# Optimization experiments

Hardware: AMD Instinct MI355X
Metric: run time of the kernel (lower is better)

Reference implementation:

```python
import jax, jax.numpy as jnp
import numpy as np

B, S, D = 2, 2048, 1024
E, K, F = 64, 6, 1408
DFF = 4096
N = B * S
CAP = 768
Z_LOSS_W = 1e-6
MOE_SCALE = 0.5  # 1/(1 + (num_shared_experts > 0))


def setup_inputs() -> dict:
    key = jax.random.key(0)
    ks = jax.random.split(key, 7)
    x = jax.random.normal(ks[0], (B, S, D), jnp.float32)
    router_w = jax.random.normal(ks[1], (E, D), jnp.float32) * 0.01
    experts_w12 = jax.random.normal(ks[2], (E, D, 2 * F), jnp.float32) * 0.011
    experts_w3 = jax.random.normal(ks[3], (E, F, D), jnp.float32) * 0.011
    gate_w = jax.random.normal(ks[4], (DFF, D), jnp.float32) * 0.011
    up_w = jax.random.normal(ks[5], (DFF, D), jnp.float32) * 0.011
    down_w = jax.random.normal(ks[6], (D, DFF), jnp.float32) * 0.011
    return {"x": x, "router_w": router_w, "experts_w12": experts_w12,
            "experts_w3": experts_w3, "gate_w": gate_w, "up_w": up_w,
            "down_w": down_w}


def reference(x, router_w, experts_w12, experts_w3, gate_w, up_w, down_w):
    b, s, d = x.shape
    h = x.reshape(-1, d)                    # [N, D]
    n = h.shape[0]

    # ---- router (fp32) ----
    logits = h @ router_w.T                 # [N, E]
    scores = jax.nn.sigmoid(logits)
    z_loss = jnp.mean(logits ** 2) * Z_LOSS_W
    # expert_bias defaults to zeros -> selection on scores directly
    _, topk_idx = jax.lax.top_k(scores, K)  # [N, K]
    topk_idx = jnp.clip(topk_idx, 0, E - 1)
    topk_logits = jnp.take_along_axis(logits, topk_idx, axis=1)
    gating = jax.nn.softmax(topk_logits, axis=-1).astype(jnp.bfloat16)  # [N, K]

    # ---- shared expert (dense SwiGLU) ----
    shared = (jax.nn.silu(h @ gate_w.T) * (h @ up_w.T)) @ down_w.T  # [N, D]

    # ---- dispatch: sort token-expert pairs by expert, scatter into padded buffer ----
    flat_idx = topk_idx.reshape(-1)                     # [N*K]
    order = jnp.argsort(flat_idx)
    expert_sorted = flat_idx[order]                     # [N*K]
    token_ids = jnp.repeat(jnp.arange(n), K)[order]     # source token per pair
    counts = jnp.bincount(flat_idx, length=E)
    starts = jnp.concatenate([jnp.zeros((1,), counts.dtype), jnp.cumsum(counts)[:-1]])
    intra = jnp.arange(n * K) - starts[expert_sorted]   # slot within expert
    valid = intra < CAP
    dest = jnp.where(valid, expert_sorted * CAP + intra, E * CAP)  # overflow -> trash row

    grouped = h[token_ids]                              # [N*K, D]
    padded = jnp.zeros((E * CAP + 1, d), h.dtype).at[dest].set(grouped)
    padded = padded[:-1].reshape(E, CAP, d)             # [E, CAP, D]

    # ---- per-expert grouped GEMM (SwiGLU) ----
    h12 = jnp.einsum('ecd,edf->ecf', padded, experts_w12)   # [E, CAP, 2F]
    h1, h2 = jnp.split(h12, 2, axis=-1)
    act = jax.nn.silu(h1) * h2
    eout = jnp.einsum('ecf,efd->ecd', act, experts_w3)      # [E, CAP, D]

    # ---- combine: gather back and scatter-add into token order ----
    eout_flat = jnp.concatenate([eout.reshape(-1, d), jnp.zeros((1, d), eout.dtype)])
    full = eout_flat[dest]                              # [N*K, D]
    g_sorted = gating.reshape(-1)[order].astype(h.dtype)
    weighted = full * g_sorted[:, None]
    routed = jnp.zeros((n, d), h.dtype).at[token_ids].add(weighted)

    # eval mode: aux_loss = 0, route_scale = 1.0
    out = (shared + routed) * MOE_SCALE
    return out.reshape(b, s, d), z_loss
```

## Files before the change

kernel.cpp:

```cpp
#include <hip/hip_runtime.h>
#include <stdint.h>
#include <math.h>

#define NTOK 4096
#define DIM  1024
#define NEXP 64
#define KSEL 6
#define FF   1408
#define FF2  2816
#define DFFC 4096
#define CAPE 768

typedef __bf16 bf16x8 __attribute__((ext_vector_type(8)));
typedef float  f32x4  __attribute__((ext_vector_type(4)));

__device__ __forceinline__ float bf2f(uint32_t h) {
  union { uint32_t u; float f; } v; v.u = h << 16; return v.f;
}
__device__ __forceinline__ uint16_t f2bf(float f) {
  union { float f; uint32_t u; } v; v.f = f;
  return (uint16_t)((v.u + 0x7fffu + ((v.u >> 16) & 1u)) >> 16);
}
__device__ __forceinline__ uint32_t pk_bf16(float a, float b) {
  uint32_t r;
  asm("v_cvt_pk_bf16_f32 %0, %1, %2" : "=v"(r) : "v"(a), "v"(b));
  return r;
}
__device__ __forceinline__ int swzh(int r) { return ((r ^ (r >> 2)) & 7) << 3; }

__device__ __forceinline__ void load_lds16(const void* g, void* l) {
  __builtin_amdgcn_global_load_lds((const __attribute__((address_space(1))) void*)g,
                                   (__attribute__((address_space(3))) void*)l, 16, 0, 0);
}

__global__ __launch_bounds__(256) void router_kernel(const float* __restrict__ x,
                                                     const float* __restrict__ rw,
                                                     int* __restrict__ topk,
                                                     uint16_t* __restrict__ gating,
                                                     float* __restrict__ tokz,
                                                     uint16_t* __restrict__ hb) {
  __shared__ float hs[16 * DIM];
  __shared__ float lg[16][NEXP];
  const int tid = threadIdx.x;
  const int t0 = blockIdx.x * 16;
  const float4* xin = (const float4*)(x + (size_t)t0 * DIM);
  float4* hs4 = (float4*)hs;
  for (int i = tid; i < 16 * DIM / 4; i += 256) hs4[i] = xin[i];
  __syncthreads();
  {
    ushort4* hbo = (ushort4*)(hb + (size_t)t0 * DIM);
    for (int i = tid; i < 16 * DIM / 4; i += 256) {
      float4 v = hs4[i];
      ushort4 o;
      o.x = f2bf(v.x); o.y = f2bf(v.y); o.z = f2bf(v.z); o.w = f2bf(v.w);
      hbo[i] = o;
    }
  }
  const int e = tid >> 2, q = tid & 3;
  float part[16];
#pragma unroll
  for (int tt = 0; tt < 16; tt++) part[tt] = 0.f;
  const float4* rw4 = (const float4*)(rw + (size_t)e * DIM + q * 256);
  for (int i = 0; i < 64; i++) {
    float4 w = rw4[i];
#pragma unroll
    for (int tt = 0; tt < 16; tt++) {
      float4 h = *(const float4*)(hs + tt * DIM + q * 256 + i * 4);
      part[tt] += h.x * w.x + h.y * w.y + h.z * w.z + h.w * w.w;
    }
  }
#pragma unroll
  for (int tt = 0; tt < 16; tt++) {
    float v = part[tt];
    v += __shfl_xor(v, 1);
    v += __shfl_xor(v, 2);
    if (q == 0) lg[tt][e] = v;
  }
  __syncthreads();
  const int wid = tid >> 6, lane = tid & 63;
  for (int ti = 0; ti < 4; ti++) {
    int tt = wid * 4 + ti;
    float v = lg[tt][lane];
    float z = v * v;
#pragma unroll
    for (int off = 32; off; off >>= 1) z += __shfl_xor(z, off);
    float bv[KSEL]; int bi[KSEL];
#pragma unroll
    for (int s = 0; s < KSEL; s++) {
      float m = v; int mi = lane;
#pragma unroll
      for (int off = 32; off; off >>= 1) {
        float om = __shfl_xor(m, off); int oi = __shfl_xor(mi, off);
        if (om > m || (om == m && oi < mi)) { m = om; mi = oi; }
      }
      bv[s] = m; bi[s] = mi;
      if (lane == mi) v = -3.0e38f;
    }
    if (lane == 0) {
      int t = t0 + tt;
      tokz[t] = z;
      float mx = bv[0];
      float ex[KSEL], sum = 0.f;
#pragma unroll
      for (int s = 0; s < KSEL; s++) { ex[s] = expf(bv[s] - mx); sum += ex[s]; }
      float inv = 1.f / sum;
#pragma unroll
      for (int s = 0; s < KSEL; s++) {
        topk[t * KSEL + s] = bi[s];
        gating[t * KSEL + s] = f2bf(ex[s] * inv);
      }
    }
  }
}

__global__ __launch_bounds__(256) void zred_kernel(const float* __restrict__ tz,
                                                   float* __restrict__ out) {
  __shared__ float s[256];
  float a = 0.f;
  for (int i = threadIdx.x; i < NTOK; i += 256) a += tz[i];
  s[threadIdx.x] = a; __syncthreads();
  for (int st = 128; st; st >>= 1) {
    if (threadIdx.x < (unsigned)st) s[threadIdx.x] += s[threadIdx.x + st];
    __syncthreads();
  }
  if (threadIdx.x == 0) out[0] = s[0] * (1e-6f / ((float)NTOK * (float)NEXP));
}

__global__ __launch_bounds__(64) void dispatch_kernel(const int* __restrict__ topk,
                                                      int* __restrict__ dest,
                                                      int* __restrict__ invmap,
                                                      int* __restrict__ counts) {
  const int e = blockIdx.x;
  const int lane = threadIdx.x;
  int base = 0;
  for (int it = 0; it < (NTOK * KSEL) / 64; it++) {
    int p = it * 64 + lane;
    int ex = topk[p];
    bool m = (ex == e);
    unsigned long long mask = __ballot(m);
    if (m) {
      int intra = base + __popcll(mask & ((1ull << lane) - 1ull));
      if (intra < CAPE) {
        dest[p] = e * CAPE + intra;
        invmap[e * CAPE + intra] = p / KSEL;
      } else {
        dest[p] = -1;
      }
    }
    base += __popcll(mask);
  }
  if (lane == 0) counts[e] = base < CAPE ? base : CAPE;
}

#define BM 128
#define BN 128
#define BKK 64

template<int EPI, int BSRC, bool IND, bool REMAP>
__global__ __launch_bounds__(256, 2) void gemm_f(const uint16_t* __restrict__ A,
                                                 const float* __restrict__ B,
                                                 const float* __restrict__ B2,
                                                 void* __restrict__ C,
                                                 const int* __restrict__ invmap,
                                                 const int* __restrict__ counts,
                                                 int K, int lda, int ldb, int ldc,
                                                 long long strideA, long long strideB,
                                                 long long strideC, int grouped,
                                                 int nM, int nN) {
  const int per = gridDim.x >> 3;
  const int w = ((int)blockIdx.x & 7) * per + ((int)blockIdx.x >> 3);
  const int mi = w % nM;
  const int q1 = w / nM;
  const int ni = q1 % nN;
  const int e  = q1 / nN;
  int cnt = 1 << 30;
  if (grouped) {
    cnt = counts[e];
    if (mi * BM >= cnt) return;
  }
  const int bm0 = mi * BM, bn0 = ni * BN;
  const uint16_t* Ab = A + (size_t)e * strideA;
  const float* Bb = B + (size_t)e * strideB;
  __shared__ alignas(16) uint16_t sA[BM * BKK];
  __shared__ alignas(16) uint16_t sB[BN * BKK];
  const int tid = threadIdx.x, wid = tid >> 6, lane = tid & 63;

  const int sa = tid >> 3;
  const int colk = (((tid & 7) ^ ((sa ^ (sa >> 2)) & 7)) * 8);
  const uint16_t* ap[4];
#pragma unroll
  for (int i = 0; i < 4; i++) {
    int row = i * 32 + sa;
    int ar = bm0 + row;
    if constexpr (IND) {
      int cr = ar < cnt ? ar : (cnt - 1);
      ar = invmap[e * CAPE + cr];
    }
    ap[i] = Ab + (size_t)ar * lda + colk;
  }

  const float* bpa = nullptr;
  const float* bpb = nullptr;
  if constexpr (BSRC == 1) {
    const int kc = (tid & 15) * 4;
    bpa = Bb + (size_t)(bn0 + (tid >> 4)) * ldb + kc;
  } else if constexpr (BSRC == 3) {
    const int kc = (tid & 15) * 4;
    const int gcol = (bn0 >> 1) + (tid >> 4);
    bpa = B  + (size_t)gcol * ldb + kc;
    bpb = B2 + (size_t)gcol * ldb + kc;
  } else {
    const int n0 = 4 * (tid & 31);
    int vn0 = bn0 + n0;
    int ng0;
    if constexpr (REMAP) {
      int blk = vn0 >> 5, lo = vn0 & 31;
      ng0 = blk * 16 + (lo & 15) + (lo < 16 ? 0 : FF);
    } else {
      ng0 = vn0;
    }
    bpa = Bb + (size_t)(4 * (tid >> 5)) * ldb + ng0;
  }

  f32x4 zero = {0.f, 0.f, 0.f, 0.f};
  f32x4 acc[4][4];
#pragma unroll
  for (int i = 0; i < 4; i++)
#pragma unroll
    for (int j = 0; j < 4; j++) acc[i][j] = zero;
  const int wm = wid >> 1, wn = wid & 1;

  for (int k0 = 0; k0 < K; k0 += BKK) {
#pragma unroll
    for (int i = 0; i < 4; i++) {
      load_lds16(ap[i], sA + i * 2048 + wid * 512);
      ap[i] += BKK;
    }
    f32x4 v[8];
    if constexpr (BSRC == 1) {
#pragma unroll
      for (int it = 0; it < 8; it++)
        v[it] = *(const f32x4*)(bpa + (size_t)(it * 16) * ldb);
      bpa += BKK;
    } else if constexpr (BSRC == 3) {
#pragma unroll
      for (int it = 0; it < 8; it++) {
        const float* s = (it & 1) ? bpb : bpa;
        v[it] = *(const f32x4*)(s + (size_t)((it >> 1) * 16) * ldb);
      }
      bpa += BKK; bpb += BKK;
    } else {
#pragma unroll
      for (int i2 = 0; i2 < 2; i2++)
#pragma unroll
        for (int j = 0; j < 4; j++)
          v[i2 * 4 + j] = *(const f32x4*)(bpa + (size_t)(32 * i2 + j) * ldb);
      bpa += (size_t)BKK * ldb;
    }
    if constexpr (BSRC == 1 || BSRC == 3) {
      const int kc = (tid & 15) * 4;
#pragma unroll
      for (int it = 0; it < 8; it++) {
        int nr = (tid >> 4) + it * 16;
        uint2 p;
        p.x = pk_bf16(v[it][0], v[it][1]);
        p.y = pk_bf16(v[it][2], v[it][3]);
        *(uint2*)(sB + nr * BKK + (kc ^ swzh(nr))) = p;
      }
    } else {
      const int n0 = 4 * (tid & 31);
#pragma unroll
      for (int i2 = 0; i2 < 2; i2++) {
        int kk0 = 4 * (tid >> 5) + 32 * i2;
#pragma unroll
        for (int c = 0; c < 4; c++) {
          int nr = n0 + c;
          uint2 p;
          p.x = pk_bf16(v[i2 * 4 + 0][c], v[i2 * 4 + 1][c]);
          p.y = pk_bf16(v[i2 * 4 + 2][c], v[i2 * 4 + 3][c]);
          *(uint2*)(sB + nr * BKK + (kk0 ^ swzh(nr))) = p;
        }
      }
    }
    __syncthreads();
#pragma unroll
    for (int ks = 0; ks < 2; ks++) {
      const int kb = ks * 32 + (lane >> 4) * 8;
      bf16x8 af[4], bfr[4];
#pragma unroll
      for (int f = 0; f < 4; f++) {
        int rowA = wm * 64 + f * 16 + (lane & 15);
        af[f] = *(const bf16x8*)(sA + rowA * BKK + (kb ^ swzh(rowA)));
      }
#pragma unroll
      for (int f = 0; f < 4; f++) {
        int rowB = wn * 64 + f * 16 + (lane & 15);
        bfr[f] = *(const bf16x8*)(sB + rowB * BKK + (kb ^ swzh(rowB)));
      }
#pragma unroll
      for (int fm = 0; fm < 4; fm++)
#pragma unroll
        for (int fn = 0; fn < 4; fn++)
          acc[fm][fn] = __builtin_amdgcn_mfma_f32_16x16x32_bf16(af[fm], bfr[fn],
                                                                acc[fm][fn], 0, 0, 0);
    }
    __syncthreads();
  }

  const int lr = (lane >> 4) * 4, lc = lane & 15;
  if constexpr (EPI == 2) {
    uint16_t* outp = (uint16_t*)C + (size_t)e * strideC;
#pragma unroll
    for (int fm = 0; fm < 4; fm++) {
#pragma unroll
      for (int fp = 0; fp < 2; fp++) {
        f32x4 g = acc[fm][2 * fp], u = acc[fm][2 * fp + 1];
        int fcol = (bn0 >> 1) + wn * 32 + fp * 16 + lc;
#pragma unroll
        for (int j = 0; j < 4; j++) {
          int r = bm0 + wm * 64 + fm * 16 + lr + j;
          float gv = g[j];
          float sv = (gv / (1.f + expf(-gv))) * u[j];
          outp[(size_t)r * ldc + fcol] = f2bf(sv);
        }
      }
    }
  } else if constexpr (EPI == 1) {
    float* outp = (float*)C + (size_t)e * strideC;
#pragma unroll
    for (int fm = 0; fm < 4; fm++)
#pragma unroll
      for (int fn = 0; fn < 4; fn++) {
        int col = bn0 + wn * 64 + fn * 16 + lc;
#pragma unroll
        for (int j = 0; j < 4; j++) {
          int r = bm0 + wm * 64 + fm * 16 + lr + j;
          outp[(size_t)r * ldc + col] = acc[fm][fn][j];
        }
      }
  } else {
    uint16_t* outp = (uint16_t*)C + (size_t)e * strideC;
#pragma unroll
    for (int fm = 0; fm < 4; fm++)
#pragma unroll
      for (int fn = 0; fn < 4; fn++) {
        int col = bn0 + wn * 64 + fn * 16 + lc;
#pragma unroll
        for (int j = 0; j < 4; j++) {
          int r = bm0 + wm * 64 + fm * 16 + lr + j;
          outp[(size_t)r * ldc + col] = f2bf(acc[fm][fn][j]);
        }
      }
  }
}

__global__ __launch_bounds__(256) void combine_kernel(const float* __restrict__ shout,
                                                      const uint16_t* __restrict__ eout,
                                                      const int* __restrict__ dest,
                                                      const uint16_t* __restrict__ gating,
                                                      float* __restrict__ out) {
  const int t = blockIdx.x;
  const int d0 = threadIdx.x * 4;
  float4 sh = *(const float4*)(shout + (size_t)t * DIM + d0);
  float rx = 0.f, ry = 0.f, rz = 0.f, rw = 0.f;
#pragma unroll
  for (int k = 0; k < KSEL; k++) {
    int dp = dest[t * KSEL + k];
    if (dp >= 0) {
      float gw = bf2f(gating[t * KSEL + k]);
      ushort4 ev = *(const ushort4*)(eout + (size_t)dp * DIM + d0);
      rx += gw * bf2f(ev.x);
      ry += gw * bf2f(ev.y);
      rz += gw * bf2f(ev.z);
      rw += gw * bf2f(ev.w);
    }
  }
  float4 o;
  o.x = (sh.x + rx) * 0.5f;
  o.y = (sh.y + ry) * 0.5f;
  o.z = (sh.z + rz) * 0.5f;
  o.w = (sh.w + rw) * 0.5f;
  *(float4*)(out + (size_t)t * DIM + d0) = o;
}

extern "C" void kernel_launch(void* const* d_in, const int* in_sizes, int n_in,
                              void* d_out, int out_size, void* d_ws, size_t ws_size,
                              hipStream_t stream) {
  (void)in_sizes; (void)n_in; (void)out_size; (void)ws_size;
  const float* x   = (const float*)d_in[0];
  const float* rw  = (const float*)d_in[1];
  const float* w12 = (const float*)d_in[2];
  const float* w3  = (const float*)d_in[3];
  const float* gw  = (const float*)d_in[4];
  const float* uw  = (const float*)d_in[5];
  const float* dw  = (const float*)d_in[6];
  float* out = (float*)d_out;

  char* ws = (char*)d_ws;
  size_t off = 0;
  auto alloc = [&](size_t sz) -> void* {
    void* p = ws + off;
    off += (sz + 255) & ~(size_t)255;
    return p;
  };
  uint16_t* HB    = (uint16_t*)alloc((size_t)NTOK * DIM * 2);
  uint16_t* S1    = (uint16_t*)alloc((size_t)NTOK * DFFC * 2);
  uint16_t* ACT   = (uint16_t*)alloc((size_t)NEXP * CAPE * FF * 2);
  uint16_t* EOUT  = (uint16_t*)alloc((size_t)NEXP * CAPE * DIM * 2);
  float* SHOUT    = (float*)alloc((size_t)NTOK * DIM * 4);
  int* TOPKB      = (int*)alloc((size_t)NTOK * KSEL * 4);
  uint16_t* GATING= (uint16_t*)alloc((size_t)NTOK * KSEL * 2);
  int* DEST       = (int*)alloc((size_t)NTOK * KSEL * 4);
  int* INVMAP     = (int*)alloc((size_t)NEXP * CAPE * 4);
  int* COUNTS     = (int*)alloc((size_t)NEXP * 4);
  float* TOKZ     = (float*)alloc((size_t)NTOK * 4);

  router_kernel<<<NTOK / 16, 256, 0, stream>>>(x, rw, TOPKB, GATING, TOKZ, HB);
  dispatch_kernel<<<NEXP, 64, 0, stream>>>(TOPKB, DEST, INVMAP, COUNTS);
  zred_kernel<<<1, 256, 0, stream>>>(TOKZ, out + (size_t)NTOK * DIM);

  gemm_f<2, 3, false, false><<<(NTOK / BM) * (2 * DFFC / BN), 256, 0, stream>>>(
      HB, gw, uw, S1, nullptr, nullptr, DIM, DIM, DIM, DFFC, 0, 0, 0, 0,
      NTOK / BM, 2 * DFFC / BN);
  gemm_f<1, 1, false, false><<<(NTOK / BM) * (DIM / BN), 256, 0, stream>>>(
      S1, dw, nullptr, SHOUT, nullptr, nullptr, DFFC, DFFC, DFFC, DIM, 0, 0, 0, 0,
      NTOK / BM, DIM / BN);

  gemm_f<2, 2, true, true><<<(CAPE / BM) * (FF2 / BN) * NEXP, 256, 0, stream>>>(
      HB, w12, nullptr, ACT, INVMAP, COUNTS, DIM, DIM, FF2, FF,
      0, (long long)DIM * FF2, (long long)CAPE * FF, 1, CAPE / BM, FF2 / BN);
  gemm_f<0, 2, false, false><<<(CAPE / BM) * (DIM / BN) * NEXP, 256, 0, stream>>>(
      ACT, w3, nullptr, EOUT, nullptr, COUNTS, FF, FF, DIM, DIM,
      (long long)CAPE * FF, (long long)FF * DIM, (long long)CAPE * DIM, 1,
      CAPE / BM, DIM / BN);

  combine_kernel<<<NTOK, 256, 0, stream>>>(SHOUT, EOUT, DEST, GATING, out);
}
```

Before: 854.0 us.

## Double-buffer LDS tiles in GEMM kernel to overlap loads with MFMA

Splits the shared-memory A and B tiles into two buffers. The next K-slice's global loads (fp32 B into registers, async A into LDS) are issued before the MFMA work on the current buffer, and B is converted and written into the other buffer afterwards. This drops one of the two barriers per iteration and hides global memory latency behind compute. The cost is twice the LDS use and more live registers, which may lower occupancy.

```diff
diff --git a/kernel.cpp b/kernel.cpp
--- a/kernel.cpp
+++ b/kernel.cpp
@@ -181,8 +181,8 @@
   const int bm0 = mi * BM, bn0 = ni * BN;
   const uint16_t* Ab = A + (size_t)e * strideA;
   const float* Bb = B + (size_t)e * strideB;
-  __shared__ alignas(16) uint16_t sA[BM * BKK];
-  __shared__ alignas(16) uint16_t sB[BN * BKK];
+  __shared__ alignas(16) uint16_t sA[2][BM * BKK];
+  __shared__ alignas(16) uint16_t sB[2][BN * BKK];
   const int tid = threadIdx.x, wid = tid >> 6, lane = tid & 63;
 
   const int sa = tid >> 3;
@@ -222,21 +222,7 @@
     bpa = Bb + (size_t)(4 * (tid >> 5)) * ldb + ng0;
   }
 
-  f32x4 zero = {0.f, 0.f, 0.f, 0.f};
-  f32x4 acc[4][4];
-#pragma unroll
-  for (int i = 0; i < 4; i++)
-#pragma unroll
-    for (int j = 0; j < 4; j++) acc[i][j] = zero;
-  const int wm = wid >> 1, wn = wid & 1;
-
-  for (int k0 = 0; k0 < K; k0 += BKK) {
-#pragma unroll
-    for (int i = 0; i < 4; i++) {
-      load_lds16(ap[i], sA + i * 2048 + wid * 512);
-      ap[i] += BKK;
-    }
-    f32x4 v[8];
+  auto loadB = [&](f32x4 (&v)[8]) {
     if constexpr (BSRC == 1) {
 #pragma unroll
       for (int it = 0; it < 8; it++)
@@ -257,6 +243,15 @@
           v[i2 * 4 + j] = *(const f32x4*)(bpa + (size_t)(32 * i2 + j) * ldb);
       bpa += (size_t)BKK * ldb;
     }
+  };
+  auto issueA = [&](int buf) {
+#pragma unroll
+    for (int i = 0; i < 4; i++) {
+      load_lds16(ap[i], sA[buf] + i * 2048 + wid * 512);
+      ap[i] += BKK;
+    }
+  };
+  auto writeB = [&](int buf, f32x4 (&v)[8]) {
     if constexpr (BSRC == 1 || BSRC == 3) {
       const int kc = (tid & 15) * 4;
 #pragma unroll
@@ -265,7 +260,7 @@
         uint2 p;
         p.x = pk_bf16(v[it][0], v[it][1]);
         p.y = pk_bf16(v[it][2], v[it][3]);
-        *(uint2*)(sB + nr * BKK + (kc ^ swzh(nr))) = p;
+        *(uint2*)(sB[buf] + nr * BKK + (kc ^ swzh(nr))) = p;
       }
     } else {
       const int n0 = 4 * (tid & 31);
@@ -278,11 +273,37 @@
           uint2 p;
           p.x = pk_bf16(v[i2 * 4 + 0][c], v[i2 * 4 + 1][c]);
           p.y = pk_bf16(v[i2 * 4 + 2][c], v[i2 * 4 + 3][c]);
-          *(uint2*)(sB + nr * BKK + (kk0 ^ swzh(nr))) = p;
+          *(uint2*)(sB[buf] + nr * BKK + (kk0 ^ swzh(nr))) = p;
         }
       }
     }
-    __syncthreads();
+  };
+
+  f32x4 zero = {0.f, 0.f, 0.f, 0.f};
+  f32x4 acc[4][4];
+#pragma unroll
+  for (int i = 0; i < 4; i++)
+#pragma unroll
+    for (int j = 0; j < 4; j++) acc[i][j] = zero;
+  const int wm = wid >> 1, wn = wid & 1;
+
+  {
+    f32x4 v[8];
+    loadB(v);
+    issueA(0);
+    writeB(0, v);
+  }
+  __syncthreads();
+
+  const int T = K / BKK;
+  for (int t = 0; t < T; t++) {
+    const int cur = t & 1;
+    const bool more = (t + 1 < T);
+    f32x4 v[8];
+    if (more) {
+      loadB(v);
+      issueA(cur ^ 1);
+    }
 #pragma unroll
     for (int ks = 0; ks < 2; ks++) {
       const int kb = ks * 32 + (lane >> 4) * 8;
@@ -290,12 +311,12 @@
 #pragma unroll
       for (int f = 0; f < 4; f++) {
         int rowA = wm * 64 + f * 16 + (lane & 15);
-        af[f] = *(const bf16x8*)(sA + rowA * BKK + (kb ^ swzh(rowA)));
+        af[f] = *(const bf16x8*)(sA[cur] + rowA * BKK + (kb ^ swzh(rowA)));
       }
 #pragma unroll
       for (int f = 0; f < 4; f++) {
         int rowB = wn * 64 + f * 16 + (lane & 15);
-        bfr[f] = *(const bf16x8*)(sB + rowB * BKK + (kb ^ swzh(rowB)));
+        bfr[f] = *(const bf16x8*)(sB[cur] + rowB * BKK + (kb ^ swzh(rowB)));
       }
 #pragma unroll
       for (int fm = 0; fm < 4; fm++)
@@ -304,6 +325,7 @@
           acc[fm][fn] = __builtin_amdgcn_mfma_f32_16x16x32_bf16(af[fm], bfr[fn],
                                                                 acc[fm][fn], 0, 0, 0);
     }
+    if (more) writeB(cur ^ 1, v);
     __syncthreads();
   }
 
```

After: 866.3 us. Within noise of the previous version (+1.4%).

## Replace GEMM with 256x256 eight-wave double-buffered phased pipeline kernel

Applied to the files above, without the earlier changes.

Replaces the 128x128, 4-wave single-buffered GEMM with a 256x256-tile, 512-thread kernel that double-buffers LDS for A and B. The K loop is split into four phases that interleave the next stage's global loads, LDS writes and async A copies with MFMA work, using barriers, waitcnt and s_setprio. The goal is more operand reuse per tile and hiding memory latency behind MFMA. In exchange, the larger LDS footprint and register use lower occupancy, and the grouped expert GEMMs waste more work on partially filled 256-row tiles.

```diff
diff --git a/kernel.cpp b/kernel.cpp
--- a/kernel.cpp
+++ b/kernel.cpp
@@ -152,21 +152,19 @@
   if (lane == 0) counts[e] = base < CAPE ? base : CAPE;
 }
 
-#define BM 128
-#define BN 128
 #define BKK 64
 
 template<int EPI, int BSRC, bool IND, bool REMAP>
-__global__ __launch_bounds__(256, 2) void gemm_f(const uint16_t* __restrict__ A,
-                                                 const float* __restrict__ B,
-                                                 const float* __restrict__ B2,
-                                                 void* __restrict__ C,
-                                                 const int* __restrict__ invmap,
-                                                 const int* __restrict__ counts,
-                                                 int K, int lda, int ldb, int ldc,
-                                                 long long strideA, long long strideB,
-                                                 long long strideC, int grouped,
-                                                 int nM, int nN) {
+__global__ __launch_bounds__(512, 2) void gemm8(const uint16_t* __restrict__ A,
+                                                const float* __restrict__ B,
+                                                const float* __restrict__ B2,
+                                                void* __restrict__ C,
+                                                const int* __restrict__ invmap,
+                                                const int* __restrict__ counts,
+                                                int K, int lda, int ldb, int ldc,
+                                                long long strideA, long long strideB,
+                                                long long strideC, int grouped,
+                                                int nM, int nN) {
   const int per = gridDim.x >> 3;
   const int w = ((int)blockIdx.x & 7) * per + ((int)blockIdx.x >> 3);
   const int mi = w % nM;
@@ -176,149 +174,212 @@
   int cnt = 1 << 30;
   if (grouped) {
     cnt = counts[e];
-    if (mi * BM >= cnt) return;
-  }
-  const int bm0 = mi * BM, bn0 = ni * BN;
+    if (mi * 256 >= cnt) return;
+  }
+  const int bm0 = mi * 256, bn0 = ni * 256;
   const uint16_t* Ab = A + (size_t)e * strideA;
   const float* Bb = B + (size_t)e * strideB;
-  __shared__ alignas(16) uint16_t sA[BM * BKK];
-  __shared__ alignas(16) uint16_t sB[BN * BKK];
+  __shared__ alignas(16) uint16_t sA[2][256 * 64];
+  __shared__ alignas(16) uint16_t sB[2][256 * 64];
   const int tid = threadIdx.x, wid = tid >> 6, lane = tid & 63;
-
-  const int sa = tid >> 3;
-  const int colk = (((tid & 7) ^ ((sa ^ (sa >> 2)) & 7)) * 8);
-  const uint16_t* ap[4];
-#pragma unroll
-  for (int i = 0; i < 4; i++) {
-    int row = i * 32 + sa;
-    int ar = bm0 + row;
-    if constexpr (IND) {
-      int cr = ar < cnt ? ar : (cnt - 1);
-      ar = invmap[e * CAPE + cr];
-    }
-    ap[i] = Ab + (size_t)ar * lda + colk;
-  }
-
-  const float* bpa = nullptr;
-  const float* bpb = nullptr;
+  const int wm = wid >> 2, wn = wid & 3;
+  const int l15 = lane & 15, q8 = (lane >> 4) * 8;
+
+  const uint16_t* apg[4];
+#pragma unroll
+  for (int h = 0; h < 2; h++)
+#pragma unroll
+    for (int i = 0; i < 2; i++) {
+      int R = h * 128 + i * 64 + (tid >> 3);
+      int ar = bm0 + R;
+      if constexpr (IND) {
+        int cr = ar < cnt ? ar : cnt - 1;
+        ar = invmap[e * CAPE + cr];
+      }
+      apg[h * 2 + i] = Ab + (size_t)ar * lda + (((tid & 7) ^ ((R ^ (R >> 2)) & 7)) * 8);
+    }
+
+  const float* bp[2];
+  long long bstep;
   if constexpr (BSRC == 1) {
-    const int kc = (tid & 15) * 4;
-    bpa = Bb + (size_t)(bn0 + (tid >> 4)) * ldb + kc;
+#pragma unroll
+    for (int h = 0; h < 2; h++) {
+      int n = bn0 + h * 128 + (tid >> 2);
+      bp[h] = Bb + (size_t)n * ldb + (tid & 3) * 16;
+    }
+    bstep = BKK;
   } else if constexpr (BSRC == 3) {
-    const int kc = (tid & 15) * 4;
-    const int gcol = (bn0 >> 1) + (tid >> 4);
-    bpa = B  + (size_t)gcol * ldb + kc;
-    bpb = B2 + (size_t)gcol * ldb + kc;
+#pragma unroll
+    for (int h = 0; h < 2; h++) {
+      int vn = bn0 + h * 128 + (tid >> 2);
+      const float* s0 = ((vn & 31) < 16) ? B : B2;
+      int pn = (vn >> 5) * 16 + (vn & 15);
+      bp[h] = s0 + (size_t)pn * ldb + (tid & 3) * 16;
+    }
+    bstep = BKK;
   } else {
-    const int n0 = 4 * (tid & 31);
-    int vn0 = bn0 + n0;
-    int ng0;
-    if constexpr (REMAP) {
-      int blk = vn0 >> 5, lo = vn0 & 31;
-      ng0 = blk * 16 + (lo & 15) + (lo < 16 ? 0 : FF);
+#pragma unroll
+    for (int h = 0; h < 2; h++) {
+      int vn0 = bn0 + h * 128 + (tid & 31) * 4;
+      int ng0;
+      if constexpr (REMAP) {
+        int blk = vn0 >> 5, lo = vn0 & 31;
+        ng0 = blk * 16 + (lo & 15) + (lo < 16 ? 0 : FF);
+      } else {
+        ng0 = vn0;
+      }
+      bp[h] = Bb + (size_t)((tid >> 5) * 4) * ldb + ng0;
+    }
+    bstep = (long long)BKK * ldb;
+  }
+
+  auto stageLoad = [&](int h, f32x4 (&bv)[4]) {
+    if constexpr (BSRC == 2) {
+#pragma unroll
+      for (int j = 0; j < 4; j++) bv[j] = *(const f32x4*)(bp[h] + (size_t)j * ldb);
     } else {
-      ng0 = vn0;
-    }
-    bpa = Bb + (size_t)(4 * (tid >> 5)) * ldb + ng0;
-  }
-
-  f32x4 zero = {0.f, 0.f, 0.f, 0.f};
-  f32x4 acc[4][4];
-#pragma unroll
-  for (int i = 0; i < 4; i++)
-#pragma unroll
-    for (int j = 0; j < 4; j++) acc[i][j] = zero;
-  const int wm = wid >> 1, wn = wid & 1;
-
-  for (int k0 = 0; k0 < K; k0 += BKK) {
-#pragma unroll
-    for (int i = 0; i < 4; i++) {
-      load_lds16(ap[i], sA + i * 2048 + wid * 512);
-      ap[i] += BKK;
-    }
-    f32x4 v[8];
-    if constexpr (BSRC == 1) {
-#pragma unroll
-      for (int it = 0; it < 8; it++)
-        v[it] = *(const f32x4*)(bpa + (size_t)(it * 16) * ldb);
-      bpa += BKK;
-    } else if constexpr (BSRC == 3) {
-#pragma unroll
-      for (int it = 0; it < 8; it++) {
-        const float* s = (it & 1) ? bpb : bpa;
-        v[it] = *(const f32x4*)(s + (size_t)((it >> 1) * 16) * ldb);
-      }
-      bpa += BKK; bpb += BKK;
+#pragma unroll
+      for (int j = 0; j < 4; j++) bv[j] = *(const f32x4*)(bp[h] + 4 * j);
+    }
+    bp[h] += bstep;
+  };
+  auto stageWrite = [&](int nb, int h, f32x4 (&bv)[4]) {
+    if constexpr (BSRC == 2) {
+#pragma unroll
+      for (int c = 0; c < 4; c++) {
+        int R = h * 128 + (tid & 31) * 4 + c;
+        uint2 p;
+        p.x = pk_bf16(bv[0][c], bv[1][c]);
+        p.y = pk_bf16(bv[2][c], bv[3][c]);
+        *(uint2*)(&sB[nb][R * 64 + (((tid >> 5) * 4) ^ swzh(R))]) = p;
+      }
     } else {
-#pragma unroll
-      for (int i2 = 0; i2 < 2; i2++)
-#pragma unroll
-        for (int j = 0; j < 4; j++)
-          v[i2 * 4 + j] = *(const f32x4*)(bpa + (size_t)(32 * i2 + j) * ldb);
-      bpa += (size_t)BKK * ldb;
-    }
-    if constexpr (BSRC == 1 || BSRC == 3) {
-      const int kc = (tid & 15) * 4;
-#pragma unroll
-      for (int it = 0; it < 8; it++) {
-        int nr = (tid >> 4) + it * 16;
-        uint2 p;
-        p.x = pk_bf16(v[it][0], v[it][1]);
-        p.y = pk_bf16(v[it][2], v[it][3]);
-        *(uint2*)(sB + nr * BKK + (kc ^ swzh(nr))) = p;
-      }
-    } else {
-      const int n0 = 4 * (tid & 31);
-#pragma unroll
-      for (int i2 = 0; i2 < 2; i2++) {
-        int kk0 = 4 * (tid >> 5) + 32 * i2;
-#pragma unroll
-        for (int c = 0; c < 4; c++) {
-          int nr = n0 + c;
-          uint2 p;
-          p.x = pk_bf16(v[i2 * 4 + 0][c], v[i2 * 4 + 1][c]);
-          p.y = pk_bf16(v[i2 * 4 + 2][c], v[i2 * 4 + 3][c]);
-          *(uint2*)(sB + nr * BKK + (kk0 ^ swzh(nr))) = p;
-        }
-      }
-    }
-    __syncthreads();
-#pragma unroll
-    for (int ks = 0; ks < 2; ks++) {
-      const int kb = ks * 32 + (lane >> 4) * 8;
-      bf16x8 af[4], bfr[4];
-#pragma unroll
-      for (int f = 0; f < 4; f++) {
-        int rowA = wm * 64 + f * 16 + (lane & 15);
-        af[f] = *(const bf16x8*)(sA + rowA * BKK + (kb ^ swzh(rowA)));
-      }
-#pragma unroll
-      for (int f = 0; f < 4; f++) {
-        int rowB = wn * 64 + f * 16 + (lane & 15);
-        bfr[f] = *(const bf16x8*)(sB + rowB * BKK + (kb ^ swzh(rowB)));
-      }
-#pragma unroll
-      for (int fm = 0; fm < 4; fm++)
-#pragma unroll
-        for (int fn = 0; fn < 4; fn++)
-          acc[fm][fn] = __builtin_amdgcn_mfma_f32_16x16x32_bf16(af[fm], bfr[fn],
-                                                                acc[fm][fn], 0, 0, 0);
-    }
-    __syncthreads();
+      int R = h * 128 + (tid >> 2);
+      int s = swzh(R);
+      uint4 u;
+      u.x = pk_bf16(bv[0][0], bv[0][1]); u.y = pk_bf16(bv[0][2], bv[0][3]);
+      u.z = pk_bf16(bv[1][0], bv[1][1]); u.w = pk_bf16(bv[1][2], bv[1][3]);
+      *(uint4*)(&sB[nb][R * 64 + ((((tid & 3) * 16) + 0) ^ s)]) = u;
+      u.x = pk_bf16(bv[2][0], bv[2][1]); u.y = pk_bf16(bv[2][2], bv[2][3]);
+      u.z = pk_bf16(bv[3][0], bv[3][1]); u.w = pk_bf16(bv[3][2], bv[3][3]);
+      *(uint4*)(&sB[nb][R * 64 + ((((tid & 3) * 16) + 8) ^ s)]) = u;
+    }
+  };
+  auto stageA = [&](int nb, int h) {
+#pragma unroll
+    for (int i = 0; i < 2; i++) {
+      load_lds16(apg[h * 2 + i], &sA[nb][h * 8192 + i * 4096 + tid * 8]);
+      apg[h * 2 + i] += BKK;
+    }
+  };
+
+  f32x4 acc[8][4];
+#pragma unroll
+  for (int i = 0; i < 8; i++)
+#pragma unroll
+    for (int j = 0; j < 4; j++) acc[i][j] = (f32x4){0.f, 0.f, 0.f, 0.f};
+
+  auto readA = [&](int buf, int mh, int ks, bf16x8 (&af)[4]) {
+#pragma unroll
+    for (int f = 0; f < 4; f++) {
+      int R = wm * 128 + (mh * 4 + f) * 16 + l15;
+      af[f] = *(const bf16x8*)(&sA[buf][R * 64 + ((ks * 32 + q8) ^ swzh(R))]);
+    }
+  };
+  auto readB = [&](int buf, int ks, bf16x8 (&bq)[4]) {
+#pragma unroll
+    for (int f = 0; f < 4; f++) {
+      int R = wn * 64 + f * 16 + l15;
+      bq[f] = *(const bf16x8*)(&sB[buf][R * 64 + ((ks * 32 + q8) ^ swzh(R))]);
+    }
+  };
+
+#define MFMAQ(mh, af, bq)                                                      \
+  _Pragma("unroll") for (int f = 0; f < 4; f++)                                \
+  _Pragma("unroll") for (int n = 0; n < 4; n++)                                \
+    acc[(mh) * 4 + f][n] = __builtin_amdgcn_mfma_f32_16x16x32_bf16(            \
+        af[f], bq[n], acc[(mh) * 4 + f][n], 0, 0, 0);
+
+#define PH_GATE()                                                              \
+  __builtin_amdgcn_s_barrier();                                                \
+  asm volatile("s_waitcnt lgkmcnt(0)" ::: "memory");                           \
+  __builtin_amdgcn_sched_barrier(0);                                           \
+  __builtin_amdgcn_s_setprio(1);
+
+#define PH_END()                                                               \
+  __builtin_amdgcn_s_setprio(0);                                               \
+  __builtin_amdgcn_s_barrier();
+
+  {
+    f32x4 bv0[4], bv1[4];
+    stageLoad(0, bv0);
+    stageLoad(1, bv1);
+    stageA(0, 0);
+    stageA(0, 1);
+    stageWrite(0, 0, bv0);
+    stageWrite(0, 1, bv1);
+  }
+  asm volatile("s_waitcnt vmcnt(0) lgkmcnt(0)" ::: "memory");
+  __builtin_amdgcn_sched_barrier(0);
+  __builtin_amdgcn_s_barrier();
+
+  const int T = K / BKK;
+  for (int t = 0; t < T; t++) {
+    const int cur = t & 1, nb = cur ^ 1;
+    const bool more = (t + 1 < T);
+    bf16x8 bq[4];
+    f32x4 bv0[4], bv1[4];
+    {
+      bf16x8 af[4];
+      readA(cur, 0, 0, af);
+      readB(cur, 0, bq);
+      if (more) stageLoad(0, bv0);
+      PH_GATE();
+      MFMAQ(0, af, bq);
+      PH_END();
+    }
+    {
+      bf16x8 af[4];
+      readA(cur, 1, 0, af);
+      if (more) { stageLoad(1, bv1); stageA(nb, 0); }
+      PH_GATE();
+      MFMAQ(1, af, bq);
+      PH_END();
+    }
+    {
+      bf16x8 af[4];
+      readA(cur, 0, 1, af);
+      readB(cur, 1, bq);
+      if (more) { stageWrite(nb, 0, bv0); stageA(nb, 1); }
+      PH_GATE();
+      MFMAQ(0, af, bq);
+      PH_END();
+    }
+    {
+      bf16x8 af[4];
+      readA(cur, 1, 1, af);
+      if (more) stageWrite(nb, 1, bv1);
+      PH_GATE();
+      MFMAQ(1, af, bq);
+      __builtin_amdgcn_s_setprio(0);
+      asm volatile("s_waitcnt vmcnt(0)" ::: "memory");
+      __builtin_amdgcn_sched_barrier(0);
+      __builtin_amdgcn_s_barrier();
+    }
   }
 
   const int lr = (lane >> 4) * 4, lc = lane & 15;
   if constexpr (EPI == 2) {
     uint16_t* outp = (uint16_t*)C + (size_t)e * strideC;
 #pragma unroll
-    for (int fm = 0; fm < 4; fm++) {
+    for (int mf = 0; mf < 8; mf++) {
 #pragma unroll
       for (int fp = 0; fp < 2; fp++) {
-        f32x4 g = acc[fm][2 * fp], u = acc[fm][2 * fp + 1];
+        f32x4 g = acc[mf][2 * fp], u = acc[mf][2 * fp + 1];
         int fcol = (bn0 >> 1) + wn * 32 + fp * 16 + lc;
 #pragma unroll
         for (int j = 0; j < 4; j++) {
-          int r = bm0 + wm * 64 + fm * 16 + lr + j;
+          int r = bm0 + wm * 128 + mf * 16 + lr + j;
           float gv = g[j];
           float sv = (gv / (1.f + expf(-gv))) * u[j];
           outp[(size_t)r * ldc + fcol] = f2bf(sv);
@@ -328,30 +389,33 @@
   } else if constexpr (EPI == 1) {
     float* outp = (float*)C + (size_t)e * strideC;
 #pragma unroll
-    for (int fm = 0; fm < 4; fm++)
-#pragma unroll
-      for (int fn = 0; fn < 4; fn++) {
-        int col = bn0 + wn * 64 + fn * 16 + lc;
+    for (int mf = 0; mf < 8; mf++)
+#pragma unroll
+      for (int nf = 0; nf < 4; nf++) {
+        int col = bn0 + wn * 64 + nf * 16 + lc;
 #pragma unroll
         for (int j = 0; j < 4; j++) {
-          int r = bm0 + wm * 64 + fm * 16 + lr + j;
-          outp[(size_t)r * ldc + col] = acc[fm][fn][j];
+          int r = bm0 + wm * 128 + mf * 16 + lr + j;
+          outp[(size_t)r * ldc + col] = acc[mf][nf][j];
         }
       }
   } else {
     uint16_t* outp = (uint16_t*)C + (size_t)e * strideC;
 #pragma unroll
-    for (int fm = 0; fm < 4; fm++)
-#pragma unroll
-      for (int fn = 0; fn < 4; fn++) {
-        int col = bn0 + wn * 64 + fn * 16 + lc;
+    for (int mf = 0; mf < 8; mf++)
+#pragma unroll
+      for (int nf = 0; nf < 4; nf++) {
+        int col = bn0 + wn * 64 + nf * 16 + lc;
 #pragma unroll
         for (int j = 0; j < 4; j++) {
-          int r = bm0 + wm * 64 + fm * 16 + lr + j;
-          outp[(size_t)r * ldc + col] = f2bf(acc[fm][fn][j]);
+          int r = bm0 + wm * 128 + mf * 16 + lr + j;
+          outp[(size_t)r * ldc + col] = f2bf(acc[mf][nf][j]);
         }
       }
   }
+#undef MFMAQ
+#undef PH_GATE
+#undef PH_END
 }
 
 __global__ __launch_bounds__(256) void combine_kernel(const float* __restrict__ shout,
@@ -419,20 +483,20 @@
   dispatch_kernel<<<NEXP, 64, 0, stream>>>(TOPKB, DEST, INVMAP, COUNTS);
   zred_kernel<<<1, 256, 0, stream>>>(TOKZ, out + (size_t)NTOK * DIM);
 
-  gemm_f<2, 3, false, false><<<(NTOK / BM) * (2 * DFFC / BN), 256, 0, stream>>>(
+  gemm8<2, 3, false, false><<<(NTOK / 256) * (2 * DFFC / 256), 512, 0, stream>>>(
       HB, gw, uw, S1, nullptr, nullptr, DIM, DIM, DIM, DFFC, 0, 0, 0, 0,
-      NTOK / BM, 2 * DFFC / BN);
-  gemm_f<1, 1, false, false><<<(NTOK / BM) * (DIM / BN), 256, 0, stream>>>(
+      NTOK / 256, 2 * DFFC / 256);
+  gemm8<1, 1, false, false><<<(NTOK / 256) * (DIM / 256), 512, 0, stream>>>(
       S1, dw, nullptr, SHOUT, nullptr, nullptr, DFFC, DFFC, DFFC, DIM, 0, 0, 0, 0,
-      NTOK / BM, DIM / BN);
-
-  gemm_f<2, 2, true, true><<<(CAPE / BM) * (FF2 / BN) * NEXP, 256, 0, stream>>>(
+      NTOK / 256, DIM / 256);
+
+  gemm8<2, 2, true, true><<<(CAPE / 256) * (FF2 / 256) * NEXP, 512, 0, stream>>>(
       HB, w12, nullptr, ACT, INVMAP, COUNTS, DIM, DIM, FF2, FF,
-      0, (long long)DIM * FF2, (long long)CAPE * FF, 1, CAPE / BM, FF2 / BN);
-  gemm_f<0, 2, false, false><<<(CAPE / BM) * (DIM / BN) * NEXP, 256, 0, stream>>>(
+      0, (long long)DIM * FF2, (long long)CAPE * FF, 1, CAPE / 256, FF2 / 256);
+  gemm8<0, 2, false, false><<<(CAPE / 256) * (DIM / 256) * NEXP, 512, 0, stream>>>(
       ACT, w3, nullptr, EOUT, nullptr, COUNTS, FF, FF, DIM, DIM,
       (long long)CAPE * FF, (long long)FF * DIM, (long long)CAPE * DIM, 1,
-      CAPE / BM, DIM / BN);
+      CAPE / 256, DIM / 256);
 
   combine_kernel<<<NTOK, 256, 0, stream>>>(SHOUT, EOUT, DEST, GATING, out);
 }
```

Measured after the change: 1.003 ms. 1.17x slower.

## Double-buffer A tiles in LDS and prefetch B into registers in GEMM

Applied to the files above, without the earlier changes.

Restructures the GEMM main loop into a software pipeline. The A tile now alternates between two LDS buffers so the next tile's global-to-LDS copy is issued before the current tile's MFMAs, and the fp32 B tile for the next step is loaded into registers while the current one is converted and stored. The __syncthreads calls become raw s_barrier plus lgkmcnt waits fenced by sched_barrier. Launch bounds go from 2 to 3 blocks per SM for more occupancy, which risks register spills given the extra prefetch registers. LDS use per block grows because of the second A buffer.

```diff
diff --git a/kernel.cpp b/kernel.cpp
--- a/kernel.cpp
+++ b/kernel.cpp
@@ -157,7 +157,7 @@
 #define BKK 64
 
 template<int EPI, int BSRC, bool IND, bool REMAP>
-__global__ __launch_bounds__(256, 2) void gemm_f(const uint16_t* __restrict__ A,
+__global__ __launch_bounds__(256, 3) void gemm_f(const uint16_t* __restrict__ A,
                                                  const float* __restrict__ B,
                                                  const float* __restrict__ B2,
                                                  void* __restrict__ C,
@@ -181,7 +181,7 @@
   const int bm0 = mi * BM, bn0 = ni * BN;
   const uint16_t* Ab = A + (size_t)e * strideA;
   const float* Bb = B + (size_t)e * strideB;
-  __shared__ alignas(16) uint16_t sA[BM * BKK];
+  __shared__ alignas(16) uint16_t sA[2][BM * BKK];
   __shared__ alignas(16) uint16_t sB[BN * BKK];
   const int tid = threadIdx.x, wid = tid >> 6, lane = tid & 63;
 
@@ -222,21 +222,7 @@
     bpa = Bb + (size_t)(4 * (tid >> 5)) * ldb + ng0;
   }
 
-  f32x4 zero = {0.f, 0.f, 0.f, 0.f};
-  f32x4 acc[4][4];
-#pragma unroll
-  for (int i = 0; i < 4; i++)
-#pragma unroll
-    for (int j = 0; j < 4; j++) acc[i][j] = zero;
-  const int wm = wid >> 1, wn = wid & 1;
-
-  for (int k0 = 0; k0 < K; k0 += BKK) {
-#pragma unroll
-    for (int i = 0; i < 4; i++) {
-      load_lds16(ap[i], sA + i * 2048 + wid * 512);
-      ap[i] += BKK;
-    }
-    f32x4 v[8];
+  auto loadB = [&](f32x4 (&v)[8]) {
     if constexpr (BSRC == 1) {
 #pragma unroll
       for (int it = 0; it < 8; it++)
@@ -257,6 +243,15 @@
           v[i2 * 4 + j] = *(const f32x4*)(bpa + (size_t)(32 * i2 + j) * ldb);
       bpa += (size_t)BKK * ldb;
     }
+  };
+  auto issueA = [&](int buf) {
+#pragma unroll
+    for (int i = 0; i < 4; i++) {
+      load_lds16(ap[i], sA[buf] + i * 2048 + wid * 512);
+      ap[i] += BKK;
+    }
+  };
+  auto writeB = [&](f32x4 (&v)[8]) {
     if constexpr (BSRC == 1 || BSRC == 3) {
       const int kc = (tid & 15) * 4;
 #pragma unroll
@@ -282,7 +277,31 @@
         }
       }
     }
-    __syncthreads();
+  };
+
+  f32x4 zero = {0.f, 0.f, 0.f, 0.f};
+  f32x4 acc[4][4];
+#pragma unroll
+  for (int i = 0; i < 4; i++)
+#pragma unroll
+    for (int j = 0; j < 4; j++) acc[i][j] = zero;
+  const int wm = wid >> 1, wn = wid & 1;
+
+  f32x4 bv[8];
+  issueA(0);
+  loadB(bv);
+
+  const int T = K / BKK;
+  for (int t = 0; t < T; t++) {
+    const int cur = t & 1, nb = cur ^ 1;
+    const bool more = (t + 1 < T);
+    if (more) issueA(nb);
+    writeB(bv);
+    if (more) loadB(bv);
+    asm volatile("s_waitcnt lgkmcnt(0)" ::: "memory");
+    __builtin_amdgcn_sched_barrier(0);
+    __builtin_amdgcn_s_barrier();
+    __builtin_amdgcn_sched_barrier(0);
 #pragma unroll
     for (int ks = 0; ks < 2; ks++) {
       const int kb = ks * 32 + (lane >> 4) * 8;
@@ -290,7 +309,7 @@
 #pragma unroll
       for (int f = 0; f < 4; f++) {
         int rowA = wm * 64 + f * 16 + (lane & 15);
-        af[f] = *(const bf16x8*)(sA + rowA * BKK + (kb ^ swzh(rowA)));
+        af[f] = *(const bf16x8*)(sA[cur] + rowA * BKK + (kb ^ swzh(rowA)));
       }
 #pragma unroll
       for (int f = 0; f < 4; f++) {
@@ -304,7 +323,9 @@
           acc[fm][fn] = __builtin_amdgcn_mfma_f32_16x16x32_bf16(af[fm], bfr[fn],
                                                                 acc[fm][fn], 0, 0, 0);
     }
-    __syncthreads();
+    __builtin_amdgcn_sched_barrier(0);
+    __builtin_amdgcn_s_barrier();
+    __builtin_amdgcn_sched_barrier(0);
   }
 
   const int lr = (lane >> 4) * 4, lc = lane & 15;
```

Result: faster. 773.6 us (-9.4%).
